# Kernel tuning notes

Measured on AMD Instinct MI355X. Metric: run time of the kernel, lower is better.

The kernel has to match this reference:

```python
import jax, jax.numpy as jnp
import numpy as np

D_MODEL = 1024
HIDDEN = 512
NUM_EXPERTS = 16
TOP_K = 2
CAP_FACTOR = 1.25
ALPHA = 0.01


def setup_inputs() -> dict:
    key = jax.random.key(0)
    ks = jax.random.split(key, 10)
    s_in = 1.0 / np.sqrt(D_MODEL)
    s_h = 1.0 / np.sqrt(HIDDEN)
    return {
        "x": jax.random.normal(ks[0], (4, 4096, D_MODEL), dtype=jnp.float32),
        "gate_w": jax.random.normal(ks[1], (D_MODEL, NUM_EXPERTS), dtype=jnp.float32) * s_in,
        "gate_b": jnp.zeros((NUM_EXPERTS,), dtype=jnp.float32),
        "gp_w": jax.random.normal(ks[2], (NUM_EXPERTS, D_MODEL, HIDDEN), dtype=jnp.float32) * s_in,
        "gp_b": jnp.zeros((NUM_EXPERTS, HIDDEN), dtype=jnp.float32),
        "up_w": jax.random.normal(ks[3], (NUM_EXPERTS, D_MODEL, HIDDEN), dtype=jnp.float32) * s_in,
        "up_b": jnp.zeros((NUM_EXPERTS, HIDDEN), dtype=jnp.float32),
        "dp_w": jax.random.normal(ks[4], (NUM_EXPERTS, HIDDEN, D_MODEL), dtype=jnp.float32) * s_h,
        "dp_b": jnp.zeros((NUM_EXPERTS, D_MODEL), dtype=jnp.float32),
    }


def reference(x, gate_w, gate_b, gp_w, gp_b, up_w, up_b, dp_w, dp_b):
    B, S, D = x.shape
    T = B * S
    xf = x.reshape(T, D)

    # --- MoEGate ---
    logits = xf @ gate_w + gate_b                      # [T, E]
    scores = jax.nn.softmax(logits, axis=-1)
    topk_w, topk_i = jax.lax.top_k(scores, TOP_K)      # [T, K]
    # norm_topk_prob=True in DeepSeekMoE
    topk_w = topk_w / (jnp.sum(topk_w, axis=-1, keepdims=True) + 1e-9)

    one_hot = jax.nn.one_hot(topk_i, NUM_EXPERTS, dtype=jnp.float32)  # [T, K, E]
    load = jnp.sum(one_hot, axis=(0, 1))               # [E]
    capacity = CAP_FACTOR * (T * TOP_K) / NUM_EXPERTS
    capacity_penalty = jnp.sum(jax.nn.relu(load - capacity)) / NUM_EXPERTS / T
    aux_loss = ALPHA * capacity_penalty

    # combine weight of expert e for each token: [T, E]
    comb = jnp.einsum("tke,tk->te", one_hot, topk_w)

    # --- dispatch/combine (dense per-expert, weighted by comb) ---
    out = jnp.zeros_like(xf)
    for e in range(NUM_EXPERTS):
        # Expert: down_proj(gate_proj(x) * silu(up_proj(x)))
        h = (xf @ gp_w[e] + gp_b[e]) * jax.nn.silu(xf @ up_w[e] + up_b[e])
        y = h @ dp_w[e] + dp_b[e]
        out = out + comb[:, e:e + 1] * y

    return out.reshape(B, S, D), aux_loss
```

## Files before the change

kernel.cpp:

```cpp
#include <hip/hip_runtime.h>
#include <hip/hip_bf16.h>
#include <math.h>

#define T_TOK 16384
#define DMODEL 1024
#define HID 512
#define NEXP 16
#define NASSIGN (T_TOK * 2)
#define HIST_BLK 64
#define TOK_PER_BLK (T_TOK / HIST_BLK)

typedef __bf16 bf16_8 __attribute__((ext_vector_type(8)));
typedef __bf16 bf16_4 __attribute__((ext_vector_type(4)));
typedef float f32_4 __attribute__((ext_vector_type(4)));

__device__ __forceinline__ void gload16(const __bf16* g, __bf16* l) {
  __builtin_amdgcn_global_load_lds(
      (const __attribute__((address_space(1))) void*)g,
      (__attribute__((address_space(3))) void*)l, 16, 0, 0);
}

__global__ __launch_bounds__(256) void gate_compute_kernel(
    const float* __restrict__ x, const float* __restrict__ gw, const float* __restrict__ gb,
    __bf16* __restrict__ xb, int* __restrict__ topk_idx, float2* __restrict__ topk_w)
{
  int wave = threadIdx.x >> 6;
  int lane = threadIdx.x & 63;
  int t = blockIdx.x * 4 + wave;
  const float* xr = x + (size_t)t * DMODEL;
  float acc[NEXP];
#pragma unroll
  for (int e = 0; e < NEXP; ++e) acc[e] = 0.f;
#pragma unroll
  for (int ii = 0; ii < DMODEL / 256; ++ii) {
    int i = ii * 256 + lane * 4;
    f32_4 xv = *(const f32_4*)(xr + i);
    bf16_4 xbv;
#pragma unroll
    for (int j = 0; j < 4; ++j) {
      xbv[j] = (__bf16)xv[j];
      const float* g = gw + (size_t)(i + j) * NEXP;
#pragma unroll
      for (int e = 0; e < NEXP; ++e) acc[e] = fmaf(xv[j], g[e], acc[e]);
    }
    *(bf16_4*)(xb + (size_t)t * DMODEL + i) = xbv;
  }
#pragma unroll
  for (int e = 0; e < NEXP; ++e) {
    float v = acc[e];
#pragma unroll
    for (int s = 32; s > 0; s >>= 1) v += __shfl_xor(v, s, 64);
    acc[e] = v;
  }
  if (lane == 0) {
    float mx = -1e30f;
#pragma unroll
    for (int e = 0; e < NEXP; ++e) { acc[e] += gb[e]; mx = fmaxf(mx, acc[e]); }
    float Z = 0.f;
#pragma unroll
    for (int e = 0; e < NEXP; ++e) { acc[e] = expf(acc[e] - mx); Z += acc[e]; }
    int i0 = 0; float s0 = acc[0];
#pragma unroll
    for (int e = 1; e < NEXP; ++e) if (acc[e] > s0) { s0 = acc[e]; i0 = e; }
    int i1 = -1; float s1 = -1e30f;
#pragma unroll
    for (int e = 0; e < NEXP; ++e) if (e != i0 && acc[e] > s1) { s1 = acc[e]; i1 = e; }
    s0 /= Z; s1 /= Z;
    float dn = s0 + s1 + 1e-9f;
    topk_idx[t] = i0 | (i1 << 8);
    topk_w[t] = make_float2(s0 / dn, s1 / dn);
  }
}

__global__ __launch_bounds__(256) void hist_kernel(
    const int* __restrict__ topk_idx, int* __restrict__ block_hist)
{
  __shared__ int cnt[NEXP];
  int tid = threadIdx.x;
  if (tid < NEXP) cnt[tid] = 0;
  __syncthreads();
  int t = blockIdx.x * TOK_PER_BLK + tid;
  int p = topk_idx[t];
  atomicAdd(&cnt[p & 0xff], 1);
  atomicAdd(&cnt[p >> 8], 1);
  __syncthreads();
  if (tid < NEXP) block_hist[blockIdx.x * NEXP + tid] = cnt[tid];
}

__global__ void scan2_kernel(const int* __restrict__ block_hist,
                             int* __restrict__ counts, int* __restrict__ offsets,
                             int* __restrict__ block_base, float* __restrict__ aux_out)
{
  __shared__ int cl[NEXP];
  int lane = threadIdx.x;
  if (lane < NEXP) {
    int s = 0;
    for (int b = 0; b < HIST_BLK; ++b) s += block_hist[b * NEXP + lane];
    cl[lane] = s;
    counts[lane] = s;
  }
  __syncthreads();
  if (lane < NEXP) {
    int off = 0;
    for (int e = 0; e < lane; ++e) off += cl[e];
    offsets[lane] = off;
    int base = off;
    for (int b = 0; b < HIST_BLK; ++b) {
      block_base[b * NEXP + lane] = base;
      base += block_hist[b * NEXP + lane];
    }
  }
  if (lane == 0) {
    int tot = 0; float pen = 0.f;
    const float cap = 1.25f * (float)(T_TOK * 2) / (float)NEXP;
    for (int e = 0; e < NEXP; ++e) {
      tot += cl[e];
      float ld = (float)cl[e] - cap;
      pen += ld > 0.f ? ld : 0.f;
    }
    offsets[NEXP] = tot;
    aux_out[0] = 0.01f * pen / (float)NEXP / (float)T_TOK;
  }
}

__global__ __launch_bounds__(256) void scatter_kernel(
    const int* __restrict__ topk_idx, const int* __restrict__ block_base,
    int* __restrict__ tok_list, int2* __restrict__ tok_slots)
{
  __shared__ int base[NEXP];
  int tid = threadIdx.x;
  if (tid < NEXP) base[tid] = block_base[blockIdx.x * NEXP + tid];
  __syncthreads();
  int t = blockIdx.x * TOK_PER_BLK + tid;
  int p = topk_idx[t];
  int i0 = p & 0xff, i1 = p >> 8;
  int p0 = atomicAdd(&base[i0], 1);
  tok_list[p0] = t;
  int p1 = atomicAdd(&base[i1], 1);
  tok_list[p1] = t;
  tok_slots[t] = make_int2(p0, p1);
}

template<int R, int C>
__global__ __launch_bounds__(256) void transpose_bf16_kernel(const float* __restrict__ in,
                                                             __bf16* __restrict__ out)
{
  __shared__ float tile[32][33];
  int e = blockIdx.z;
  int c0 = blockIdx.x * 32, r0 = blockIdx.y * 32;
  const float* src = in + ((size_t)e * R + r0) * C + c0;
#pragma unroll
  for (int i = 0; i < 4; ++i) {
    int r = threadIdx.y + i * 8;
    tile[r][threadIdx.x] = src[(size_t)r * C + threadIdx.x];
  }
  __syncthreads();
  __bf16* dst = out + ((size_t)e * C + c0) * R + r0;
#pragma unroll
  for (int i = 0; i < 4; ++i) {
    int c = threadIdx.y + i * 8;
    dst[(size_t)c * R + threadIdx.x] = (__bf16)tile[threadIdx.x][c];
  }
}


__device__ __forceinline__ void ffn1_tile(const __bf16* As, const __bf16* Bgs, const __bf16* Bus,
                                          int wave, int l16, int quad,
                                          f32_4 accg[2][4], f32_4 accu[2][4])
{
  bf16_8 af[2];
#pragma unroll
  for (int mb = 0; mb < 2; ++mb)
    af[mb] = *(const bf16_8*)(As + (wave * 32 + mb * 16 + l16) * 32 + quad * 8);
#pragma unroll
  for (int nb = 0; nb < 4; ++nb) {
    bf16_8 bg = *(const bf16_8*)(Bgs + (nb * 16 + l16) * 32 + quad * 8);
    bf16_8 bu = *(const bf16_8*)(Bus + (nb * 16 + l16) * 32 + quad * 8);
#pragma unroll
    for (int mb = 0; mb < 2; ++mb) {
      accg[mb][nb] = __builtin_amdgcn_mfma_f32_16x16x32_bf16(af[mb], bg, accg[mb][nb], 0, 0, 0);
      accu[mb][nb] = __builtin_amdgcn_mfma_f32_16x16x32_bf16(af[mb], bu, accu[mb][nb], 0, 0, 0);
    }
  }
}

__global__ __launch_bounds__(256) void ffn1_kernel(
    const __bf16* __restrict__ xb, const __bf16* __restrict__ gpb, const __bf16* __restrict__ upb,
    const float* __restrict__ gp_b, const float* __restrict__ up_b,
    const int* __restrict__ counts, const int* __restrict__ offsets,
    const int* __restrict__ tok_list, __bf16* __restrict__ h)
{
  int e = blockIdx.z;
  int cnt = counts[e];
  int m0 = blockIdx.y * 128;
  if (m0 >= cnt) return;
  int n0 = blockIdx.x * 64;
  int offe = offsets[e];

  __shared__ __align__(16) __bf16 As[2][128 * 32];
  __shared__ __align__(16) __bf16 Bgs[2][64 * 32];
  __shared__ __align__(16) __bf16 Bus[2][64 * 32];
  __shared__ int toks[128];

  int tid = threadIdx.x;
  if (tid < 128) {
    int r = m0 + tid;
    toks[tid] = tok_list[offe + (r < cnt ? r : cnt - 1)];
  }
  __syncthreads();

  int wave = tid >> 6, lane = tid & 63;
  int quad = lane >> 4, l16 = lane & 15;
  int rr = tid >> 2, ko = (tid & 3) * 8;

  const __bf16* ga0 = xb + (size_t)toks[rr] * DMODEL + ko;
  const __bf16* ga1 = xb + (size_t)toks[64 + rr] * DMODEL + ko;
  const __bf16* gbg = gpb + ((size_t)e * HID + n0 + rr) * DMODEL + ko;
  const __bf16* gbu = upb + ((size_t)e * HID + n0 + rr) * DMODEL + ko;

  f32_4 accg[2][4], accu[2][4];
  {
    f32_4 z = {0.f, 0.f, 0.f, 0.f};
#pragma unroll
    for (int a = 0; a < 2; ++a)
#pragma unroll
      for (int b = 0; b < 4; ++b) { accg[a][b] = z; accu[a][b] = z; }
  }

  gload16(ga0, &As[0][tid * 8]);
  gload16(ga1, &As[0][(256 + tid) * 8]);
  gload16(gbg, &Bgs[0][tid * 8]);
  gload16(gbu, &Bus[0][tid * 8]);
  __syncthreads();

  int cur = 0;
  for (int k0 = 0; k0 < DMODEL - 32; k0 += 32) {
    int nxt = cur ^ 1;
    gload16(ga0 + k0 + 32, &As[nxt][tid * 8]);
    gload16(ga1 + k0 + 32, &As[nxt][(256 + tid) * 8]);
    gload16(gbg + k0 + 32, &Bgs[nxt][tid * 8]);
    gload16(gbu + k0 + 32, &Bus[nxt][tid * 8]);
    ffn1_tile(As[cur], Bgs[cur], Bus[cur], wave, l16, quad, accg, accu);
    __syncthreads();
    cur = nxt;
  }
  ffn1_tile(As[cur], Bgs[cur], Bus[cur], wave, l16, quad, accg, accu);

#pragma unroll
  for (int mb = 0; mb < 2; ++mb)
#pragma unroll
    for (int nb = 0; nb < 4; ++nb)
#pragma unroll
      for (int rg = 0; rg < 4; ++rg) {
        int row = wave * 32 + mb * 16 + quad * 4 + rg;
        int r = m0 + row;
        if (r < cnt) {
          int n = n0 + nb * 16 + l16;
          float g = accg[mb][nb][rg] + gp_b[e * HID + n];
          float u = accu[mb][nb][rg] + up_b[e * HID + n];
          float sw = u / (1.f + expf(-u));
          h[(size_t)(offe + r) * HID + n] = (__bf16)(g * sw);
        }
      }
}

__device__ __forceinline__ void ffn2_tile(const __bf16* As, const __bf16* Bs,
                                          int wave, int l16, int quad, f32_4 acc[2][8])
{
  bf16_8 af[2];
#pragma unroll
  for (int mb = 0; mb < 2; ++mb)
    af[mb] = *(const bf16_8*)(As + (wave * 32 + mb * 16 + l16) * 32 + quad * 8);
#pragma unroll
  for (int nb = 0; nb < 8; ++nb) {
    bf16_8 bb = *(const bf16_8*)(Bs + (nb * 16 + l16) * 32 + quad * 8);
#pragma unroll
    for (int mb = 0; mb < 2; ++mb)
      acc[mb][nb] = __builtin_amdgcn_mfma_f32_16x16x32_bf16(af[mb], bb, acc[mb][nb], 0, 0, 0);
  }
}

__global__ __launch_bounds__(256) void ffn2_kernel(
    const __bf16* __restrict__ h, const __bf16* __restrict__ dpb, const float* __restrict__ dp_b,
    const int* __restrict__ counts, const int* __restrict__ offsets,
    __bf16* __restrict__ ybuf)
{
  int e = blockIdx.z;
  int cnt = counts[e];
  int m0 = blockIdx.y * 128;
  if (m0 >= cnt) return;
  int n0 = blockIdx.x * 128;
  int offe = offsets[e];

  __shared__ __align__(16) __bf16 As[2][128 * 32];
  __shared__ __align__(16) __bf16 Bs[2][128 * 32];

  int tid = threadIdx.x;
  int wave = tid >> 6, lane = tid & 63;
  int quad = lane >> 4, l16 = lane & 15;
  int rr = tid >> 2, ko = (tid & 3) * 8;

  int ra0 = m0 + rr;        if (ra0 >= cnt) ra0 = cnt - 1;
  int ra1 = m0 + 64 + rr;   if (ra1 >= cnt) ra1 = cnt - 1;
  const __bf16* ga0 = h + (size_t)(offe + ra0) * HID + ko;
  const __bf16* ga1 = h + (size_t)(offe + ra1) * HID + ko;
  const __bf16* gb0 = dpb + ((size_t)e * DMODEL + n0 + rr) * HID + ko;
  const __bf16* gb1 = dpb + ((size_t)e * DMODEL + n0 + 64 + rr) * HID + ko;

  f32_4 acc[2][8];
  {
    f32_4 z = {0.f, 0.f, 0.f, 0.f};
#pragma unroll
    for (int a = 0; a < 2; ++a)
#pragma unroll
      for (int b = 0; b < 8; ++b) acc[a][b] = z;
  }

  gload16(ga0, &As[0][tid * 8]);
  gload16(ga1, &As[0][(256 + tid) * 8]);
  gload16(gb0, &Bs[0][tid * 8]);
  gload16(gb1, &Bs[0][(256 + tid) * 8]);
  __syncthreads();

  int cur = 0;
  for (int k0 = 0; k0 < HID - 32; k0 += 32) {
    int nxt = cur ^ 1;
    gload16(ga0 + k0 + 32, &As[nxt][tid * 8]);
    gload16(ga1 + k0 + 32, &As[nxt][(256 + tid) * 8]);
    gload16(gb0 + k0 + 32, &Bs[nxt][tid * 8]);
    gload16(gb1 + k0 + 32, &Bs[nxt][(256 + tid) * 8]);
    ffn2_tile(As[cur], Bs[cur], wave, l16, quad, acc);
    __syncthreads();
    cur = nxt;
  }
  ffn2_tile(As[cur], Bs[cur], wave, l16, quad, acc);

#pragma unroll
  for (int mb = 0; mb < 2; ++mb)
#pragma unroll
    for (int nb = 0; nb < 8; ++nb)
#pragma unroll
      for (int rg = 0; rg < 4; ++rg) {
        int row = wave * 32 + mb * 16 + quad * 4 + rg;
        int r = m0 + row;
        if (r < cnt) {
          int n = n0 + nb * 16 + l16;
          float v = acc[mb][nb][rg] + dp_b[e * DMODEL + n];
          ybuf[(size_t)(offe + r) * DMODEL + n] = (__bf16)v;
        }
      }
}

__global__ __launch_bounds__(256) void combine_kernel(
    const __bf16* __restrict__ ybuf, const int2* __restrict__ tok_slots,
    const float2* __restrict__ topk_w, float* __restrict__ out)
{
  int tid = threadIdx.x;
  int t = blockIdx.x * 2 + (tid >> 7);
  int d = (tid & 127) * 8;
  int2 sl = tok_slots[t];
  float2 w = topk_w[t];
  bf16_8 y0 = *(const bf16_8*)(ybuf + (size_t)sl.x * DMODEL + d);
  bf16_8 y1 = *(const bf16_8*)(ybuf + (size_t)sl.y * DMODEL + d);
  float* o = out + (size_t)t * DMODEL + d;
  f32_4 r0, r1;
#pragma unroll
  for (int i = 0; i < 4; ++i) r0[i] = w.x * (float)y0[i] + w.y * (float)y1[i];
#pragma unroll
  for (int i = 0; i < 4; ++i) r1[i] = w.x * (float)y0[4 + i] + w.y * (float)y1[4 + i];
  *(f32_4*)o = r0;
  *(f32_4*)(o + 4) = r1;
}

extern "C" void kernel_launch(void* const* d_in, const int* in_sizes, int n_in,
                              void* d_out, int out_size, void* d_ws, size_t ws_size,
                              hipStream_t stream)
{
  const float* x      = (const float*)d_in[0];
  const float* gate_w = (const float*)d_in[1];
  const float* gate_b = (const float*)d_in[2];
  const float* gp_w   = (const float*)d_in[3];
  const float* gp_b   = (const float*)d_in[4];
  const float* up_w   = (const float*)d_in[5];
  const float* up_b   = (const float*)d_in[6];
  const float* dp_w   = (const float*)d_in[7];
  const float* dp_b   = (const float*)d_in[8];

  char* ws = (char*)d_ws;
  size_t o = 0;
  __bf16* xb  = (__bf16*)(ws + o); o += (size_t)T_TOK * DMODEL * 2;
  __bf16* gpb = (__bf16*)(ws + o); o += (size_t)NEXP * DMODEL * HID * 2;
  __bf16* upb = (__bf16*)(ws + o); o += (size_t)NEXP * DMODEL * HID * 2;
  __bf16* dpb = (__bf16*)(ws + o); o += (size_t)NEXP * HID * DMODEL * 2;
  __bf16* hbuf = (__bf16*)(ws + o); o += (size_t)NASSIGN * HID * 2;
  int*   tok_list = (int*)(ws + o); o += (size_t)NASSIGN * 4;
  int2*  tok_slots = (int2*)(ws + o); o += (size_t)T_TOK * 8;
  int*   topk_idx = (int*)(ws + o); o += (size_t)T_TOK * 4;
  float2* topk_w  = (float2*)(ws + o); o += (size_t)T_TOK * 8;
  int*   block_hist = (int*)(ws + o); o += (size_t)HIST_BLK * NEXP * 4;
  int*   block_base = (int*)(ws + o); o += (size_t)HIST_BLK * NEXP * 4;
  int*   counts   = (int*)(ws + o); o += 64;
  int*   offsets  = (int*)(ws + o); o += 128;
  __bf16* ybuf = (__bf16*)ws;

  float* out = (float*)d_out;
  float* aux = out + (size_t)T_TOK * DMODEL;

  gate_compute_kernel<<<T_TOK / 4, 256, 0, stream>>>(x, gate_w, gate_b, xb, topk_idx, topk_w);
  hist_kernel<<<HIST_BLK, TOK_PER_BLK, 0, stream>>>(topk_idx, block_hist);
  scan2_kernel<<<1, 64, 0, stream>>>(block_hist, counts, offsets, block_base, aux);
  scatter_kernel<<<HIST_BLK, TOK_PER_BLK, 0, stream>>>(topk_idx, block_base, tok_list, tok_slots);
  transpose_bf16_kernel<DMODEL, HID><<<dim3(HID / 32, DMODEL / 32, NEXP), dim3(32, 8), 0, stream>>>(gp_w, gpb);
  transpose_bf16_kernel<DMODEL, HID><<<dim3(HID / 32, DMODEL / 32, NEXP), dim3(32, 8), 0, stream>>>(up_w, upb);
  transpose_bf16_kernel<HID, DMODEL><<<dim3(DMODEL / 32, HID / 32, NEXP), dim3(32, 8), 0, stream>>>(dp_w, dpb);
  ffn1_kernel<<<dim3(HID / 64, T_TOK / 128, NEXP), 256, 0, stream>>>(xb, gpb, upb, gp_b, up_b,
                                                                     counts, offsets, tok_list, hbuf);
  ffn2_kernel<<<dim3(DMODEL / 128, T_TOK / 128, NEXP), 256, 0, stream>>>(hbuf, dpb, dp_b,
                                                                         counts, offsets, ybuf);
  combine_kernel<<<T_TOK / 2, 256, 0, stream>>>(ybuf, tok_slots, topk_w, out);
}
```

Measured before the change: 558.2 us.

## Enlarge expert GEMM tiles to 256x256 with interleaved gate/up weights

Measured after the change: 590.9 us. 5.8% more time.

```diff
diff --git a/kernel.cpp b/kernel.cpp
--- a/kernel.cpp
+++ b/kernel.cpp
@@ -141,214 +141,259 @@
   tok_slots[t] = make_int2(p0, p1);
 }
 
-template<int R, int C>
-__global__ __launch_bounds__(256) void transpose_bf16_kernel(const float* __restrict__ in,
-                                                             __bf16* __restrict__ out)
+__global__ __launch_bounds__(256) void transpose_w1_kernel(const float* __restrict__ gp,
+                                                           const float* __restrict__ up,
+                                                           __bf16* __restrict__ wb1)
+{
+  __shared__ float tile[32][33];
+  int ez = blockIdx.z;
+  int e = ez >> 1, isup = ez & 1;
+  const float* in = isup ? up : gp;
+  int c0 = blockIdx.x * 32, r0 = blockIdx.y * 32;
+  const float* src = in + ((size_t)e * 1024 + r0) * 512 + c0;
+#pragma unroll
+  for (int i = 0; i < 4; ++i) {
+    int r = threadIdx.y + i * 8;
+    tile[r][threadIdx.x] = src[(size_t)r * 512 + threadIdx.x];
+  }
+  __syncthreads();
+#pragma unroll
+  for (int i = 0; i < 4; ++i) {
+    int cc = threadIdx.y + i * 8;
+    int np = 2 * c0 + 2 * (cc & ~15) + (cc & 15) + 16 * isup;
+    wb1[((size_t)e * 1024 + np) * 1024 + r0 + threadIdx.x] = (__bf16)tile[threadIdx.x][cc];
+  }
+}
+
+__global__ __launch_bounds__(256) void transpose_dp_kernel(const float* __restrict__ in,
+                                                           __bf16* __restrict__ out)
 {
   __shared__ float tile[32][33];
   int e = blockIdx.z;
   int c0 = blockIdx.x * 32, r0 = blockIdx.y * 32;
-  const float* src = in + ((size_t)e * R + r0) * C + c0;
+  const float* src = in + ((size_t)e * 512 + r0) * 1024 + c0;
 #pragma unroll
   for (int i = 0; i < 4; ++i) {
     int r = threadIdx.y + i * 8;
-    tile[r][threadIdx.x] = src[(size_t)r * C + threadIdx.x];
-  }
-  __syncthreads();
-  __bf16* dst = out + ((size_t)e * C + c0) * R + r0;
+    tile[r][threadIdx.x] = src[(size_t)r * 1024 + threadIdx.x];
+  }
+  __syncthreads();
+  __bf16* dst = out + ((size_t)e * 1024 + c0) * 512 + r0;
 #pragma unroll
   for (int i = 0; i < 4; ++i) {
     int c = threadIdx.y + i * 8;
-    dst[(size_t)c * R + threadIdx.x] = (__bf16)tile[threadIdx.x][c];
-  }
-}
-
-
-__device__ __forceinline__ void ffn1_tile(const __bf16* As, const __bf16* Bgs, const __bf16* Bus,
-                                          int wave, int l16, int quad,
-                                          f32_4 accg[2][4], f32_4 accu[2][4])
-{
-  bf16_8 af[2];
-#pragma unroll
-  for (int mb = 0; mb < 2; ++mb)
-    af[mb] = *(const bf16_8*)(As + (wave * 32 + mb * 16 + l16) * 32 + quad * 8);
-#pragma unroll
-  for (int nb = 0; nb < 4; ++nb) {
-    bf16_8 bg = *(const bf16_8*)(Bgs + (nb * 16 + l16) * 32 + quad * 8);
-    bf16_8 bu = *(const bf16_8*)(Bus + (nb * 16 + l16) * 32 + quad * 8);
-#pragma unroll
-    for (int mb = 0; mb < 2; ++mb) {
-      accg[mb][nb] = __builtin_amdgcn_mfma_f32_16x16x32_bf16(af[mb], bg, accg[mb][nb], 0, 0, 0);
-      accu[mb][nb] = __builtin_amdgcn_mfma_f32_16x16x32_bf16(af[mb], bu, accu[mb][nb], 0, 0, 0);
-    }
-  }
-}
-
-__global__ __launch_bounds__(256) void ffn1_kernel(
-    const __bf16* __restrict__ xb, const __bf16* __restrict__ gpb, const __bf16* __restrict__ upb,
+    dst[(size_t)c * 512 + threadIdx.x] = (__bf16)tile[threadIdx.x][c];
+  }
+}
+
+
+__global__ __launch_bounds__(512, 2) void ffn1_kernel(
+    const __bf16* __restrict__ xb, const __bf16* __restrict__ wb1,
     const float* __restrict__ gp_b, const float* __restrict__ up_b,
     const int* __restrict__ counts, const int* __restrict__ offsets,
     const int* __restrict__ tok_list, __bf16* __restrict__ h)
 {
   int e = blockIdx.z;
   int cnt = counts[e];
-  int m0 = blockIdx.y * 128;
+  int m0 = blockIdx.y * 256;
   if (m0 >= cnt) return;
-  int n0 = blockIdx.x * 64;
+  int n0 = blockIdx.x * 256;
   int offe = offsets[e];
 
-  __shared__ __align__(16) __bf16 As[2][128 * 32];
-  __shared__ __align__(16) __bf16 Bgs[2][64 * 32];
-  __shared__ __align__(16) __bf16 Bus[2][64 * 32];
-  __shared__ int toks[128];
+  __shared__ __align__(16) __bf16 As[2][256 * 64];
+  __shared__ __align__(16) __bf16 Bs[2][256 * 64];
+  __shared__ int toks[256];
 
   int tid = threadIdx.x;
-  if (tid < 128) {
+  if (tid < 256) {
     int r = m0 + tid;
     toks[tid] = tok_list[offe + (r < cnt ? r : cnt - 1)];
   }
   __syncthreads();
 
-  int wave = tid >> 6, lane = tid & 63;
-  int quad = lane >> 4, l16 = lane & 15;
-  int rr = tid >> 2, ko = (tid & 3) * 8;
-
-  const __bf16* ga0 = xb + (size_t)toks[rr] * DMODEL + ko;
-  const __bf16* ga1 = xb + (size_t)toks[64 + rr] * DMODEL + ko;
-  const __bf16* gbg = gpb + ((size_t)e * HID + n0 + rr) * DMODEL + ko;
-  const __bf16* gbu = upb + ((size_t)e * HID + n0 + rr) * DMODEL + ko;
-
-  f32_4 accg[2][4], accu[2][4];
+  int rr = tid >> 3, ko = (tid & 7) * 8;
+  const __bf16* ga[4];
+  const __bf16* gb[4];
+#pragma unroll
+  for (int i = 0; i < 4; ++i) {
+    ga[i] = xb + (size_t)toks[i * 64 + rr] * DMODEL + ko;
+    gb[i] = wb1 + ((size_t)e * 1024 + n0 + i * 64 + rr) * DMODEL + ko;
+  }
+
+  int wid = tid >> 6;
+  int wr = wid >> 2, wc = wid & 3;
+  int lane = tid & 63, quad = lane >> 4, l16 = lane & 15;
+
+  f32_4 acc[8][4];
   {
     f32_4 z = {0.f, 0.f, 0.f, 0.f};
 #pragma unroll
-    for (int a = 0; a < 2; ++a)
-#pragma unroll
-      for (int b = 0; b < 4; ++b) { accg[a][b] = z; accu[a][b] = z; }
-  }
-
-  gload16(ga0, &As[0][tid * 8]);
-  gload16(ga1, &As[0][(256 + tid) * 8]);
-  gload16(gbg, &Bgs[0][tid * 8]);
-  gload16(gbu, &Bus[0][tid * 8]);
-  __syncthreads();
-
+    for (int a = 0; a < 8; ++a)
+#pragma unroll
+      for (int b = 0; b < 4; ++b) acc[a][b] = z;
+  }
+
+#define FFN1_STAGE(buf, kt)                                         \
+  {                                                                 \
+    int k0_ = (kt) * 64;                                            \
+    _Pragma("unroll")                                               \
+    for (int i = 0; i < 4; ++i) {                                   \
+      gload16(ga[i] + k0_, &As[buf][(tid + i * 512) * 8]);          \
+      gload16(gb[i] + k0_, &Bs[buf][(tid + i * 512) * 8]);          \
+    }                                                               \
+  }
+
+#define FFN1_COMP(buf)                                                               \
+  {                                                                                  \
+    const __bf16* A_ = As[buf];                                                      \
+    const __bf16* B_ = Bs[buf];                                                      \
+    _Pragma("unroll")                                                                \
+    for (int ks = 0; ks < 2; ++ks) {                                                 \
+      bf16_8 bf[4];                                                                  \
+      _Pragma("unroll")                                                              \
+      for (int ni = 0; ni < 4; ++ni)                                                 \
+        bf[ni] = *(const bf16_8*)(B_ + (wc * 64 + ni * 16 + l16) * 64 + ks * 32 + quad * 8); \
+      _Pragma("unroll")                                                              \
+      for (int mi = 0; mi < 8; ++mi) {                                               \
+        bf16_8 af = *(const bf16_8*)(A_ + (wr * 128 + mi * 16 + l16) * 64 + ks * 32 + quad * 8); \
+        _Pragma("unroll")                                                            \
+        for (int ni = 0; ni < 4; ++ni)                                               \
+          acc[mi][ni] = __builtin_amdgcn_mfma_f32_16x16x32_bf16(af, bf[ni], acc[mi][ni], 0, 0, 0); \
+      }                                                                              \
+    }                                                                                \
+  }
+
+  FFN1_STAGE(0, 0);
+  __syncthreads();
   int cur = 0;
-  for (int k0 = 0; k0 < DMODEL - 32; k0 += 32) {
-    int nxt = cur ^ 1;
-    gload16(ga0 + k0 + 32, &As[nxt][tid * 8]);
-    gload16(ga1 + k0 + 32, &As[nxt][(256 + tid) * 8]);
-    gload16(gbg + k0 + 32, &Bgs[nxt][tid * 8]);
-    gload16(gbu + k0 + 32, &Bus[nxt][tid * 8]);
-    ffn1_tile(As[cur], Bgs[cur], Bus[cur], wave, l16, quad, accg, accu);
+  for (int kt = 0; kt < DMODEL / 64 - 1; ++kt) {
+    FFN1_STAGE(cur ^ 1, kt + 1);
+    FFN1_COMP(cur);
     __syncthreads();
-    cur = nxt;
-  }
-  ffn1_tile(As[cur], Bgs[cur], Bus[cur], wave, l16, quad, accg, accu);
-
-#pragma unroll
-  for (int mb = 0; mb < 2; ++mb)
-#pragma unroll
-    for (int nb = 0; nb < 4; ++nb)
+    cur ^= 1;
+  }
+  FFN1_COMP(cur);
+
+#pragma unroll
+  for (int mi = 0; mi < 8; ++mi)
+#pragma unroll
+    for (int j = 0; j < 2; ++j) {
+      int c = (n0 >> 1) + wc * 32 + j * 16 + l16;
+      float gbias = gp_b[e * HID + c];
+      float ubias = up_b[e * HID + c];
 #pragma unroll
       for (int rg = 0; rg < 4; ++rg) {
-        int row = wave * 32 + mb * 16 + quad * 4 + rg;
-        int r = m0 + row;
+        int r = m0 + wr * 128 + mi * 16 + quad * 4 + rg;
         if (r < cnt) {
-          int n = n0 + nb * 16 + l16;
-          float g = accg[mb][nb][rg] + gp_b[e * HID + n];
-          float u = accu[mb][nb][rg] + up_b[e * HID + n];
+          float g = acc[mi][2 * j][rg] + gbias;
+          float u = acc[mi][2 * j + 1][rg] + ubias;
           float sw = u / (1.f + expf(-u));
-          h[(size_t)(offe + r) * HID + n] = (__bf16)(g * sw);
+          h[(size_t)(offe + r) * HID + c] = (__bf16)(g * sw);
         }
       }
-}
-
-__device__ __forceinline__ void ffn2_tile(const __bf16* As, const __bf16* Bs,
-                                          int wave, int l16, int quad, f32_4 acc[2][8])
-{
-  bf16_8 af[2];
-#pragma unroll
-  for (int mb = 0; mb < 2; ++mb)
-    af[mb] = *(const bf16_8*)(As + (wave * 32 + mb * 16 + l16) * 32 + quad * 8);
-#pragma unroll
-  for (int nb = 0; nb < 8; ++nb) {
-    bf16_8 bb = *(const bf16_8*)(Bs + (nb * 16 + l16) * 32 + quad * 8);
-#pragma unroll
-    for (int mb = 0; mb < 2; ++mb)
-      acc[mb][nb] = __builtin_amdgcn_mfma_f32_16x16x32_bf16(af[mb], bb, acc[mb][nb], 0, 0, 0);
-  }
-}
-
-__global__ __launch_bounds__(256) void ffn2_kernel(
+    }
+#undef FFN1_STAGE
+#undef FFN1_COMP
+}
+
+__global__ __launch_bounds__(512, 2) void ffn2_kernel(
     const __bf16* __restrict__ h, const __bf16* __restrict__ dpb, const float* __restrict__ dp_b,
     const int* __restrict__ counts, const int* __restrict__ offsets,
     __bf16* __restrict__ ybuf)
 {
   int e = blockIdx.z;
   int cnt = counts[e];
-  int m0 = blockIdx.y * 128;
+  int m0 = blockIdx.y * 256;
   if (m0 >= cnt) return;
-  int n0 = blockIdx.x * 128;
+  int n0 = blockIdx.x * 256;
   int offe = offsets[e];
 
-  __shared__ __align__(16) __bf16 As[2][128 * 32];
-  __shared__ __align__(16) __bf16 Bs[2][128 * 32];
+  __shared__ __align__(16) __bf16 As[2][256 * 64];
+  __shared__ __align__(16) __bf16 Bs[2][256 * 64];
 
   int tid = threadIdx.x;
-  int wave = tid >> 6, lane = tid & 63;
-  int quad = lane >> 4, l16 = lane & 15;
-  int rr = tid >> 2, ko = (tid & 3) * 8;
-
-  int ra0 = m0 + rr;        if (ra0 >= cnt) ra0 = cnt - 1;
-  int ra1 = m0 + 64 + rr;   if (ra1 >= cnt) ra1 = cnt - 1;
-  const __bf16* ga0 = h + (size_t)(offe + ra0) * HID + ko;
-  const __bf16* ga1 = h + (size_t)(offe + ra1) * HID + ko;
-  const __bf16* gb0 = dpb + ((size_t)e * DMODEL + n0 + rr) * HID + ko;
-  const __bf16* gb1 = dpb + ((size_t)e * DMODEL + n0 + 64 + rr) * HID + ko;
-
-  f32_4 acc[2][8];
+  int rr = tid >> 3, ko = (tid & 7) * 8;
+  const __bf16* ga[4];
+  const __bf16* gb[4];
+#pragma unroll
+  for (int i = 0; i < 4; ++i) {
+    int r = m0 + i * 64 + rr;
+    if (r >= cnt) r = cnt - 1;
+    ga[i] = h + (size_t)(offe + r) * HID + ko;
+    gb[i] = dpb + ((size_t)e * DMODEL + n0 + i * 64 + rr) * HID + ko;
+  }
+
+  int wid = tid >> 6;
+  int wr = wid >> 2, wc = wid & 3;
+  int lane = tid & 63, quad = lane >> 4, l16 = lane & 15;
+
+  f32_4 acc[8][4];
   {
     f32_4 z = {0.f, 0.f, 0.f, 0.f};
 #pragma unroll
-    for (int a = 0; a < 2; ++a)
-#pragma unroll
-      for (int b = 0; b < 8; ++b) acc[a][b] = z;
-  }
-
-  gload16(ga0, &As[0][tid * 8]);
-  gload16(ga1, &As[0][(256 + tid) * 8]);
-  gload16(gb0, &Bs[0][tid * 8]);
-  gload16(gb1, &Bs[0][(256 + tid) * 8]);
-  __syncthreads();
-
+    for (int a = 0; a < 8; ++a)
+#pragma unroll
+      for (int b = 0; b < 4; ++b) acc[a][b] = z;
+  }
+
+#define FFN2_STAGE(buf, kt)                                         \
+  {                                                                 \
+    int k0_ = (kt) * 64;                                            \
+    _Pragma("unroll")                                               \
+    for (int i = 0; i < 4; ++i) {                                   \
+      gload16(ga[i] + k0_, &As[buf][(tid + i * 512) * 8]);          \
+      gload16(gb[i] + k0_, &Bs[buf][(tid + i * 512) * 8]);          \
+    }                                                               \
+  }
+
+#define FFN2_COMP(buf)                                                               \
+  {                                                                                  \
+    const __bf16* A_ = As[buf];                                                      \
+    const __bf16* B_ = Bs[buf];                                                      \
+    _Pragma("unroll")                                                                \
+    for (int ks = 0; ks < 2; ++ks) {                                                 \
+      bf16_8 bf[4];                                                                  \
+      _Pragma("unroll")                                                              \
+      for (int ni = 0; ni < 4; ++ni)                                                 \
+        bf[ni] = *(const bf16_8*)(B_ + (wc * 64 + ni * 16 + l16) * 64 + ks * 32 + quad * 8); \
+      _Pragma("unroll")                                                              \
+      for (int mi = 0; mi < 8; ++mi) {                                               \
+        bf16_8 af = *(const bf16_8*)(A_ + (wr * 128 + mi * 16 + l16) * 64 + ks * 32 + quad * 8); \
+        _Pragma("unroll")                                                            \
+        for (int ni = 0; ni < 4; ++ni)                                               \
+          acc[mi][ni] = __builtin_amdgcn_mfma_f32_16x16x32_bf16(af, bf[ni], acc[mi][ni], 0, 0, 0); \
+      }                                                                              \
+    }                                                                                \
+  }
+
+  FFN2_STAGE(0, 0);
+  __syncthreads();
   int cur = 0;
-  for (int k0 = 0; k0 < HID - 32; k0 += 32) {
-    int nxt = cur ^ 1;
-    gload16(ga0 + k0 + 32, &As[nxt][tid * 8]);
-    gload16(ga1 + k0 + 32, &As[nxt][(256 + tid) * 8]);
-    gload16(gb0 + k0 + 32, &Bs[nxt][tid * 8]);
-    gload16(gb1 + k0 + 32, &Bs[nxt][(256 + tid) * 8]);
-    ffn2_tile(As[cur], Bs[cur], wave, l16, quad, acc);
+  for (int kt = 0; kt < HID / 64 - 1; ++kt) {
+    FFN2_STAGE(cur ^ 1, kt + 1);
+    FFN2_COMP(cur);
     __syncthreads();
-    cur = nxt;
-  }
-  ffn2_tile(As[cur], Bs[cur], wave, l16, quad, acc);
-
-#pragma unroll
-  for (int mb = 0; mb < 2; ++mb)
-#pragma unroll
-    for (int nb = 0; nb < 8; ++nb)
+    cur ^= 1;
+  }
+  FFN2_COMP(cur);
+
+#pragma unroll
+  for (int mi = 0; mi < 8; ++mi)
+#pragma unroll
+    for (int ni = 0; ni < 4; ++ni) {
+      int n = n0 + wc * 64 + ni * 16 + l16;
+      float bias = dp_b[e * DMODEL + n];
 #pragma unroll
       for (int rg = 0; rg < 4; ++rg) {
-        int row = wave * 32 + mb * 16 + quad * 4 + rg;
-        int r = m0 + row;
+        int r = m0 + wr * 128 + mi * 16 + quad * 4 + rg;
         if (r < cnt) {
-          int n = n0 + nb * 16 + l16;
-          float v = acc[mb][nb][rg] + dp_b[e * DMODEL + n];
+          float v = acc[mi][ni][rg] + bias;
           ybuf[(size_t)(offe + r) * DMODEL + n] = (__bf16)v;
         }
       }
+    }
+#undef FFN2_STAGE
+#undef FFN2_COMP
 }
 
 __global__ __launch_bounds__(256) void combine_kernel(
@@ -389,9 +434,8 @@
   char* ws = (char*)d_ws;
   size_t o = 0;
   __bf16* xb  = (__bf16*)(ws + o); o += (size_t)T_TOK * DMODEL * 2;
-  __bf16* gpb = (__bf16*)(ws + o); o += (size_t)NEXP * DMODEL * HID * 2;
-  __bf16* upb = (__bf16*)(ws + o); o += (size_t)NEXP * DMODEL * HID * 2;
-  __bf16* dpb = (__bf16*)(ws + o); o += (size_t)NEXP * HID * DMODEL * 2;
+  __bf16* wb1 = (__bf16*)(ws + o); o += (size_t)NEXP * 1024 * DMODEL * 2;
+  __bf16* dpb = (__bf16*)(ws + o); o += (size_t)NEXP * DMODEL * HID * 2;
   __bf16* hbuf = (__bf16*)(ws + o); o += (size_t)NASSIGN * HID * 2;
   int*   tok_list = (int*)(ws + o); o += (size_t)NASSIGN * 4;
   int2*  tok_slots = (int2*)(ws + o); o += (size_t)T_TOK * 8;
@@ -410,12 +454,11 @@
   hist_kernel<<<HIST_BLK, TOK_PER_BLK, 0, stream>>>(topk_idx, block_hist);
   scan2_kernel<<<1, 64, 0, stream>>>(block_hist, counts, offsets, block_base, aux);
   scatter_kernel<<<HIST_BLK, TOK_PER_BLK, 0, stream>>>(topk_idx, block_base, tok_list, tok_slots);
-  transpose_bf16_kernel<DMODEL, HID><<<dim3(HID / 32, DMODEL / 32, NEXP), dim3(32, 8), 0, stream>>>(gp_w, gpb);
-  transpose_bf16_kernel<DMODEL, HID><<<dim3(HID / 32, DMODEL / 32, NEXP), dim3(32, 8), 0, stream>>>(up_w, upb);
-  transpose_bf16_kernel<HID, DMODEL><<<dim3(DMODEL / 32, HID / 32, NEXP), dim3(32, 8), 0, stream>>>(dp_w, dpb);
-  ffn1_kernel<<<dim3(HID / 64, T_TOK / 128, NEXP), 256, 0, stream>>>(xb, gpb, upb, gp_b, up_b,
-                                                                     counts, offsets, tok_list, hbuf);
-  ffn2_kernel<<<dim3(DMODEL / 128, T_TOK / 128, NEXP), 256, 0, stream>>>(hbuf, dpb, dp_b,
-                                                                         counts, offsets, ybuf);
+  transpose_w1_kernel<<<dim3(512 / 32, 1024 / 32, 2 * NEXP), dim3(32, 8), 0, stream>>>(gp_w, up_w, wb1);
+  transpose_dp_kernel<<<dim3(1024 / 32, 512 / 32, NEXP), dim3(32, 8), 0, stream>>>(dp_w, dpb);
+  ffn1_kernel<<<dim3(1024 / 256, NASSIGN / 256, NEXP), 512, 0, stream>>>(xb, wb1, gp_b, up_b,
+                                                                         counts, offsets, tok_list, hbuf);
+  ffn2_kernel<<<dim3(DMODEL / 256, NASSIGN / 256, NEXP), 512, 0, stream>>>(hbuf, dpb, dp_b,
+                                                                           counts, offsets, ybuf);
   combine_kernel<<<T_TOK / 2, 256, 0, stream>>>(ybuf, tok_slots, topk_w, out);
 }
```
